# Kernel optimization log

Hardware: AMD Instinct MI355X
Metric: run time of the kernel (lower is better)

The kernel has to match this reference:

```python
import jax, jax.numpy as jnp
import numpy as np

B = 131072
D = 64
NUM_REL = 32


def setup_inputs() -> dict:
    key = jax.random.key(0)
    k1, k2, k3, k4 = jax.random.split(key, 4)
    embeds1 = jax.random.normal(k1, (B, D), dtype=jnp.float32)
    embeds2 = jax.random.normal(k2, (B, D), dtype=jnp.float32)
    rels = jax.random.randint(k3, (B,), 0, NUM_REL, dtype=jnp.int32)
    # learned relation table: one D*D matrix per relation type
    rel_embeds = jax.random.normal(k4, (NUM_REL, D * D), dtype=jnp.float32)
    return {"embeds1": embeds1, "embeds2": embeds2, "rels": rels,
            "rel_embeds": rel_embeds}


def reference(embeds1, embeds2, rels, rel_embeds):
    # gather per-sample relation matrices: [B, D, D]
    rel_mats = rel_embeds[rels].reshape(-1, D, D)
    # per-sample bilinear form: score_b = e1_b^T R_b e2_b  -> [B]
    e1R = jnp.einsum("bd,bde->be", embeds1, rel_mats)
    return (e1R * embeds2).sum(axis=1)
```

## Files before the change

kernel.cpp:

```cpp
#include <hip/hip_runtime.h>
#include <hip/hip_bf16.h>
#include <cstddef>

#define BB 131072
#define DD 64
#define NREL 32

#define CAP 4608
#define SPW 32
#define SPB 128
#define BLKX (CAP / SPB)
#define PERM_SLOTS (NREL * CAP)

#define SCB 256
#define SCT 512
#define CSTRIDE 16

#define RSTR 72

typedef __attribute__((ext_vector_type(8))) __bf16 bf16x8;
typedef __attribute__((ext_vector_type(16))) float f32x16;

__global__ __launch_bounds__(SCT) void scatter_atomic(
    const int* __restrict__ rels, int* __restrict__ cursor,
    int* __restrict__ perm) {
  __shared__ int hist[NREL];
  __shared__ int base[NREL];
  const int t = threadIdx.x;
  if (t < NREL) hist[t] = 0;
  __syncthreads();
  const int s = blockIdx.x * SCT + t;
  const int rv = rels[s];
  const int rank = atomicAdd(&hist[rv], 1);
  __syncthreads();
  if (t < NREL) base[t] = atomicAdd(&cursor[t * CSTRIDE], hist[t]);
  __syncthreads();
  perm[rv * CAP + base[rv] + rank] = s;
}

__global__ __launch_bounds__(256, 4) void bilinear_mfma(
    const float* __restrict__ e1g, const float* __restrict__ e2g,
    const float* __restrict__ relE, const int* __restrict__ perm,
    const int* __restrict__ cursor, float* __restrict__ out) {
  __shared__ float smem[4608];
  __bf16* RH = (__bf16*)smem;
  __bf16* RL = RH + 64 * RSTR;
  const int t = threadIdx.x;
  const int r0 = blockIdx.y;
  const int end = cursor[r0 * CSTRIDE];
  const int sbBlk = blockIdx.x * SPB;
  if (sbBlk >= end) return;

  const int wid = t >> 6;
  const int lane = t & 63;
  const int h = lane >> 5;
  const int l31 = lane & 31;
  const int slot = sbBlk + wid * SPW + l31;
  const bool valid = (slot < end) & (h == 0);
  const int pk = perm[r0 * CAP + slot] & 0x1FFFF;

  float a[4][8];
  {
    const float* rowp = e1g + (size_t)pk * DD + 8 * h;
#pragma unroll
    for (int kc = 0; kc < 4; ++kc) {
      const float4 x0 = *(const float4*)(rowp + kc * 16);
      const float4 x1 = *(const float4*)(rowp + kc * 16 + 4);
      a[kc][0] = x0.x; a[kc][1] = x0.y; a[kc][2] = x0.z; a[kc][3] = x0.w;
      a[kc][4] = x1.x; a[kc][5] = x1.y; a[kc][6] = x1.z; a[kc][7] = x1.w;
    }
  }

  {
    const float* Rg = relE + (size_t)r0 * (DD * DD);
    const int k = t >> 2;
    const int n0 = (t & 3) * 16;
    float4 x[4];
#pragma unroll
    for (int i = 0; i < 4; ++i)
      x[i] = *(const float4*)(Rg + (size_t)k * DD + n0 + 4 * i);
    const float* xs = (const float*)x;
#pragma unroll
    for (int j = 0; j < 16; ++j) {
      const float v = xs[j];
      const __bf16 hb = (__bf16)v;
      RH[(n0 + j) * RSTR + k] = hb;
      RL[(n0 + j) * RSTR + k] = (__bf16)(v - (float)hb);
    }
  }
  __syncthreads();

  f32x16 acc[2];
#pragma unroll
  for (int tj = 0; tj < 2; ++tj)
#pragma unroll
    for (int i = 0; i < 16; ++i) acc[tj][i] = 0.f;

#pragma unroll
  for (int kc = 0; kc < 4; ++kc) {
    bf16x8 aH, aL;
#pragma unroll
    for (int j = 0; j < 8; ++j) {
      const __bf16 hb = (__bf16)a[kc][j];
      aH[j] = hb;
      aL[j] = (__bf16)(a[kc][j] - (float)hb);
    }
#pragma unroll
    for (int tj = 0; tj < 2; ++tj) {
      const int bo = (32 * tj + l31) * RSTR + kc * 16 + 8 * h;
      const bf16x8 bH = *(const bf16x8*)(RH + bo);
      const bf16x8 bL = *(const bf16x8*)(RL + bo);
      acc[tj] = __builtin_amdgcn_mfma_f32_32x32x16_bf16(aH, bH, acc[tj], 0, 0, 0);
      acc[tj] = __builtin_amdgcn_mfma_f32_32x32x16_bf16(aH, bL, acc[tj], 0, 0, 0);
      acc[tj] = __builtin_amdgcn_mfma_f32_32x32x16_bf16(aL, bH, acc[tj], 0, 0, 0);
    }
  }

  __syncthreads();

  float* sP = smem + wid * (SPW * 33);
#pragma unroll
  for (int g = 0; g < 4; ++g)
#pragma unroll
    for (int q = 0; q < 4; ++q) {
      const int reg = g * 4 + q;
      const int rbase = q + 8 * g;
      const int s0 = __builtin_amdgcn_readlane(pk, rbase);
      const int s1 = __builtin_amdgcn_readlane(pk, rbase + 4);
      const int bs = h ? s1 : s0;
      const float* er = e2g + (size_t)bs * DD + l31;
      const float v = fmaf(acc[0][reg], er[0], acc[1][reg] * er[32]);
      sP[(rbase + 4 * h) * 33 + l31] = v;
    }
  __syncthreads();
  float sc = 0.f;
#pragma unroll
  for (int c = 0; c < 16; ++c) sc += sP[l31 * 33 + 16 * h + c];
  sc += __shfl_xor(sc, 32);
  if (valid) out[pk] = sc;
}

extern "C" void kernel_launch(void* const* d_in, const int* in_sizes, int n_in,
                              void* d_out, int out_size, void* d_ws, size_t ws_size,
                              hipStream_t stream) {
  const float* e1 = (const float*)d_in[0];
  const float* e2 = (const float*)d_in[1];
  const int* rels = (const int*)d_in[2];
  const float* relE = (const float*)d_in[3];
  float* out = (float*)d_out;

  int* perm = (int*)d_ws;
  int* cursor = perm + PERM_SLOTS;

  hipMemsetAsync(cursor, 0, NREL * CSTRIDE * sizeof(int), stream);
  scatter_atomic<<<SCB, SCT, 0, stream>>>(rels, cursor, perm);
  bilinear_mfma<<<dim3(BLKX, NREL), 256, 0, stream>>>(e1, e2, relE, perm,
                                                      cursor, out);
}
```

Before: 108.6 us.

## Compute per-sample dot with e2 via a second MFMA and extract the diagonal

The per-sample dot product with embeds2 is no longer done with scattered per-element global loads in the epilogue. e2 rows are loaded coalesced into registers alongside e1, the e1·R tile is staged in shared memory, and a second split-bf16 MFMA forms the 32x32 product of the staged tile with e2. Only the diagonal of that product is kept, picked out with a lane shuffle. This removes the gathered e2 reads and the shared-memory reduction loop, but spends 32x redundant MFMA work, adds bf16-split rounding error on the intermediate, and needs more shared memory.

```diff
diff --git a/kernel.cpp b/kernel.cpp
--- a/kernel.cpp
+++ b/kernel.cpp
@@ -17,6 +17,7 @@
 #define CSTRIDE 16
 
 #define RSTR 72
+#define SPSTR 65
 
 typedef __attribute__((ext_vector_type(8))) __bf16 bf16x8;
 typedef __attribute__((ext_vector_type(16))) float f32x16;
@@ -42,7 +43,7 @@
     const float* __restrict__ e1g, const float* __restrict__ e2g,
     const float* __restrict__ relE, const int* __restrict__ perm,
     const int* __restrict__ cursor, float* __restrict__ out) {
-  __shared__ float smem[4608];
+  __shared__ float smem[4 * SPW * SPSTR];
   __bf16* RH = (__bf16*)smem;
   __bf16* RL = RH + 64 * RSTR;
   const int t = threadIdx.x;
@@ -90,6 +91,18 @@
   }
   __syncthreads();
 
+  float e2v[4][8];
+  {
+    const float* rowp = e2g + (size_t)pk * DD + 8 * h;
+#pragma unroll
+    for (int kc = 0; kc < 4; ++kc) {
+      const float4 x0 = *(const float4*)(rowp + kc * 16);
+      const float4 x1 = *(const float4*)(rowp + kc * 16 + 4);
+      e2v[kc][0] = x0.x; e2v[kc][1] = x0.y; e2v[kc][2] = x0.z; e2v[kc][3] = x0.w;
+      e2v[kc][4] = x1.x; e2v[kc][5] = x1.y; e2v[kc][6] = x1.z; e2v[kc][7] = x1.w;
+    }
+  }
+
   f32x16 acc[2];
 #pragma unroll
   for (int tj = 0; tj < 2; ++tj)
@@ -118,25 +131,43 @@
 
   __syncthreads();
 
-  float* sP = smem + wid * (SPW * 33);
+  float* sP = smem + wid * (SPW * SPSTR);
 #pragma unroll
   for (int g = 0; g < 4; ++g)
 #pragma unroll
     for (int q = 0; q < 4; ++q) {
-      const int reg = g * 4 + q;
-      const int rbase = q + 8 * g;
-      const int s0 = __builtin_amdgcn_readlane(pk, rbase);
-      const int s1 = __builtin_amdgcn_readlane(pk, rbase + 4);
-      const int bs = h ? s1 : s0;
-      const float* er = e2g + (size_t)bs * DD + l31;
-      const float v = fmaf(acc[0][reg], er[0], acc[1][reg] * er[32]);
-      sP[(rbase + 4 * h) * 33 + l31] = v;
+      const int row = q + 8 * g + 4 * h;
+#pragma unroll
+      for (int tj = 0; tj < 2; ++tj)
+        sP[row * SPSTR + 32 * tj + l31] = acc[tj][g * 4 + q];
     }
-  __syncthreads();
-  float sc = 0.f;
+
+  f32x16 acc2;
 #pragma unroll
-  for (int c = 0; c < 16; ++c) sc += sP[l31 * 33 + 16 * h + c];
-  sc += __shfl_xor(sc, 32);
+  for (int i = 0; i < 16; ++i) acc2[i] = 0.f;
+#pragma unroll
+  for (int kc = 0; kc < 4; ++kc) {
+    const float* pr = &sP[l31 * SPSTR + kc * 16 + 8 * h];
+    bf16x8 pH, pL, eH, eL;
+#pragma unroll
+    for (int j = 0; j < 8; ++j) {
+      const float pv = pr[j];
+      const __bf16 phb = (__bf16)pv;
+      pH[j] = phb;
+      pL[j] = (__bf16)(pv - (float)phb);
+      const float ev = e2v[kc][j];
+      const __bf16 ehb = (__bf16)ev;
+      eH[j] = ehb;
+      eL[j] = (__bf16)(ev - (float)ehb);
+    }
+    acc2 = __builtin_amdgcn_mfma_f32_32x32x16_bf16(pH, eH, acc2, 0, 0, 0);
+    acc2 = __builtin_amdgcn_mfma_f32_32x32x16_bf16(pH, eL, acc2, 0, 0, 0);
+    acc2 = __builtin_amdgcn_mfma_f32_32x32x16_bf16(pL, eH, acc2, 0, 0, 0);
+  }
+
+  const float mine = acc2[(l31 & 3) + 4 * (l31 >> 3)];
+  const float theirs = __shfl_xor(mine, 32);
+  const float sc = (((l31 >> 2) & 1) == h) ? mine : theirs;
   if (valid) out[pk] = sc;
 }
 
```

Result: no change. 110.5 us (+1.8%).
